# Kernel optimization log

Hardware: AMD Instinct MI355X
Metric: run time of the kernel (lower is better)

Reference implementation:

```python
import jax, jax.numpy as jnp
import numpy as np


def setup_inputs() -> dict:
    key = jax.random.key(0)
    ks = jax.random.split(key, 6)
    B, HW, CIN, COUT, K = 256, 64, 3, 128, 32
    inputs = jax.random.normal(ks[0], (B, HW, HW, CIN), jnp.float32)
    conv_w = jax.random.normal(ks[1], (3, 3, CIN, COUT), jnp.float32) * 0.1
    conv_b = jnp.zeros((COUT,), jnp.float32)
    match_w = jax.random.normal(ks[2], (COUT,), jnp.float32) * 0.1
    match_b = jnp.zeros((1,), jnp.float32)
    pat_w = jax.random.normal(ks[3], (32 * 32 * K, 1), jnp.float32) * 0.01
    pat_b = jnp.zeros((1,), jnp.float32)
    base_w = jax.random.normal(ks[4], (32 * 32 * COUT, 3), jnp.float32) * 0.01
    base_b = jnp.zeros((3,), jnp.float32)
    pattern_set_index = jax.random.randint(ks[5], (K,), 0, COUT, jnp.int32)
    return {
        "inputs": inputs, "conv_w": conv_w, "conv_b": conv_b,
        "match_w": match_w, "match_b": match_b,
        "pat_w": pat_w, "pat_b": pat_b,
        "base_w": base_w, "base_b": base_b,
        "pattern_set_index": pattern_set_index,
    }


def reference(inputs, conv_w, conv_b, match_w, match_b,
              pat_w, pat_b, base_w, base_b, pattern_set_index):
    B = inputs.shape[0]
    # feat_extract: conv3x3 stride 2 + relu -> feats0 [B,32,32,128]; GAP -> feats1 [B,128]
    feats0 = jax.nn.relu(
        jax.lax.conv_general_dilated(
            inputs, conv_w, window_strides=(2, 2), padding='SAME',
            dimension_numbers=('NHWC', 'HWIO', 'NHWC')) + conv_b)
    feats1 = feats0.mean(axis=(1, 2))  # [B,128]
    # pat_matcher: boolean per-sample match mask
    matches = (feats1 @ match_w + match_b[0]) > 0.0  # [B] bool
    # pat_pred on channel-subset features (tf.gather axis=3)
    sel = jnp.take(feats0, pattern_set_index, axis=3)  # [B,32,32,32]
    p = jax.nn.sigmoid(sel.reshape(B, -1) @ pat_w + pat_b)[:, 0]  # [B]
    # BinaryToCategorical(pattern_class=0, num_classes=3): [p, (1-p)/2, (1-p)/2]
    o = (1.0 - p) * 0.5
    cat = jnp.stack([p, o, o], axis=-1)  # [B,3]
    # base_pred on full features (used for matched-low and non-matched samples)
    base = jax.nn.softmax(feats0.reshape(B, -1) @ base_w + base_b, axis=-1)  # [B,3]
    # route: matched AND pat score >= 0.5 -> categorized pat pred, else base pred
    use_pat = matches & (p >= 0.5)
    return jnp.where(use_pat[:, None], cat, base)
```

## Files before the change

### kernel.cpp

```cpp
#include <hip/hip_runtime.h>
#include <math.h>

#define TPB 512

__global__ __launch_bounds__(TPB, 2)
void pattern_branch_kernel(const float* __restrict__ in,
                           const float* __restrict__ conv_w,
                           const float* __restrict__ conv_b,
                           const float* __restrict__ match_w,
                           const float* __restrict__ match_b,
                           const float* __restrict__ pat_w,
                           const float* __restrict__ pat_b,
                           const float* __restrict__ base_w,
                           const float* __restrict__ base_b,
                           const int*   __restrict__ psi,
                           float* __restrict__ out)
{
    constexpr int ROWF4 = 50;
    constexpr int ROWF  = 200;
    __shared__ float4 xlds4[65 * ROWF4];
    __shared__ float  red[8][5];

    const float* xlds = (const float*)xlds4;
    const int b   = blockIdx.x;
    const int tid = threadIdx.x;

    for (int s = tid; s < 65 * ROWF4; s += TPB) xlds4[s] = make_float4(0.f, 0.f, 0.f, 0.f);
    __syncthreads();
    const float4* inp4 = (const float4*)(in + (size_t)b * 12288);
    for (int s = tid; s < 64 * 48; s += TPB) {
        int r = s / 48;
        int q = s - r * 48;
        xlds4[r * ROWF4 + q] = inp4[s];
    }
    __syncthreads();

    const int lane31 = tid & 31;
    const int grp    = tid >> 5;
    float w[4][27], bias[4], mw[4];
    #pragma unroll
    for (int j = 0; j < 4; ++j) {
        int c = lane31 + 32 * j;
        bias[j] = conv_b[c];
        mw[j]   = match_w[c];
        #pragma unroll
        for (int k = 0; k < 27; ++k) w[j][k] = conv_w[k * 128 + c];
    }

    float s_match = 0.f, sb0 = 0.f, sb1 = 0.f, sb2 = 0.f;

    for (int it = 0; it < 16; ++it) {
        int slot = it * 16 + grp;
        int oh = slot >> 3;
        int q  = slot & 7;
        float acc[4][4];
        #pragma unroll
        for (int v = 0; v < 4; ++v)
            #pragma unroll
            for (int j = 0; j < 4; ++j) acc[v][j] = bias[j];

        #pragma unroll
        for (int kh = 0; kh < 3; ++kh) {
            float xr[28];
            const float4* rp = &xlds4[(2 * oh + kh) * ROWF4 + 6 * q];
            #pragma unroll
            for (int u = 0; u < 7; ++u) {
                float4 v4 = rp[u];
                xr[4*u] = v4.x; xr[4*u+1] = v4.y; xr[4*u+2] = v4.z; xr[4*u+3] = v4.w;
            }
            #pragma unroll
            for (int v = 0; v < 4; ++v)
                #pragma unroll
                for (int t9 = 0; t9 < 9; ++t9) {
                    float xv = xr[6 * v + t9];
                    int k = kh * 9 + t9;
                    acc[v][0] = fmaf(xv, w[0][k], acc[v][0]);
                    acc[v][1] = fmaf(xv, w[1][k], acc[v][1]);
                    acc[v][2] = fmaf(xv, w[2][k], acc[v][2]);
                    acc[v][3] = fmaf(xv, w[3][k], acc[v][3]);
                }
        }
        #pragma unroll
        for (int v = 0; v < 4; ++v) {
            int hw = oh * 32 + 4 * q + v;
            const float* bp = base_w + (size_t)(hw * 128 + lane31) * 3;
            #pragma unroll
            for (int j = 0; j < 4; ++j) {
                float fv = fmaxf(acc[v][j], 0.f);
                s_match = fmaf(mw[j], fv, s_match);
                const float* bpj = bp + j * 96;
                sb0 = fmaf(fv, bpj[0], sb0);
                sb1 = fmaf(fv, bpj[1], sb1);
                sb2 = fmaf(fv, bpj[2], sb2);
            }
        }
    }

    float s_pat = 0.f;
    {
        const int lane8 = tid & 7;
        const int pgrp  = tid >> 3;
        int pk[4];
        float pbias[4];
        float pw[4][27];
        #pragma unroll
        for (int j = 0; j < 4; ++j) {
            int k = lane8 + 8 * j;
            pk[j] = k;
            int c = psi[k];
            pbias[j] = conv_b[c];
            #pragma unroll
            for (int kk = 0; kk < 27; ++kk) pw[j][kk] = conv_w[kk * 128 + c];
        }
        for (int it = 0; it < 16; ++it) {
            int hw = it * 64 + pgrp;
            int oh = hw >> 5, ow = hw & 31;
            float a0 = pbias[0], a1 = pbias[1], a2 = pbias[2], a3 = pbias[3];
            #pragma unroll
            for (int kh = 0; kh < 3; ++kh) {
                float xr[10];
                const float2* rp = (const float2*)(xlds + (2 * oh + kh) * ROWF) + 3 * ow;
                #pragma unroll
                for (int u = 0; u < 5; ++u) { float2 v2 = rp[u]; xr[2*u] = v2.x; xr[2*u+1] = v2.y; }
                #pragma unroll
                for (int t9 = 0; t9 < 9; ++t9) {
                    float xv = xr[t9];
                    int k = kh * 9 + t9;
                    a0 = fmaf(xv, pw[0][k], a0);
                    a1 = fmaf(xv, pw[1][k], a1);
                    a2 = fmaf(xv, pw[2][k], a2);
                    a3 = fmaf(xv, pw[3][k], a3);
                }
            }
            const float* pwp = pat_w + hw * 32;
            s_pat = fmaf(fmaxf(a0, 0.f), pwp[pk[0]], s_pat);
            s_pat = fmaf(fmaxf(a1, 0.f), pwp[pk[1]], s_pat);
            s_pat = fmaf(fmaxf(a2, 0.f), pwp[pk[2]], s_pat);
            s_pat = fmaf(fmaxf(a3, 0.f), pwp[pk[3]], s_pat);
        }
    }

    float vals[5] = { s_match, sb0, sb1, sb2, s_pat };
    #pragma unroll
    for (int off = 32; off > 0; off >>= 1)
        #pragma unroll
        for (int v = 0; v < 5; ++v)
            vals[v] += __shfl_down(vals[v], off, 64);
    int wv = tid >> 6, lane = tid & 63;
    if (lane == 0) {
        #pragma unroll
        for (int v = 0; v < 5; ++v) red[wv][v] = vals[v];
    }
    __syncthreads();
    if (tid == 0) {
        float t[5] = {0.f, 0.f, 0.f, 0.f, 0.f};
        for (int wj = 0; wj < 8; ++wj)
            #pragma unroll
            for (int v = 0; v < 5; ++v) t[v] += red[wj][v];
        float score = t[0] * (1.f / 1024.f) + match_b[0];
        float p = 1.f / (1.f + expf(-(t[4] + pat_b[0])));
        float l0 = t[1] + base_b[0], l1 = t[2] + base_b[1], l2 = t[3] + base_b[2];
        float m = fmaxf(l0, fmaxf(l1, l2));
        float e0 = expf(l0 - m), e1 = expf(l1 - m), e2 = expf(l2 - m);
        float inv = 1.f / (e0 + e1 + e2);
        bool use_pat = (score > 0.f) && (p >= 0.5f);
        float o0, o1, o2;
        if (use_pat) { o0 = p; o1 = 0.5f * (1.f - p); o2 = o1; }
        else         { o0 = e0 * inv; o1 = e1 * inv; o2 = e2 * inv; }
        out[b * 3 + 0] = o0;
        out[b * 3 + 1] = o1;
        out[b * 3 + 2] = o2;
    }
}

extern "C" void kernel_launch(void* const* d_in, const int* in_sizes, int n_in,
                              void* d_out, int out_size, void* d_ws, size_t ws_size,
                              hipStream_t stream) {
    const float* in      = (const float*)d_in[0];
    const float* conv_w  = (const float*)d_in[1];
    const float* conv_b  = (const float*)d_in[2];
    const float* match_w = (const float*)d_in[3];
    const float* match_b = (const float*)d_in[4];
    const float* pat_w   = (const float*)d_in[5];
    const float* pat_b   = (const float*)d_in[6];
    const float* base_w  = (const float*)d_in[7];
    const float* base_b  = (const float*)d_in[8];
    const int*   psi     = (const int*)d_in[9];
    float* out = (float*)d_out;

    int B = in_sizes[0] / (64 * 64 * 3);
    pattern_branch_kernel<<<B, TPB, 0, stream>>>(
        in, conv_w, conv_b, match_w, match_b, pat_w, pat_b,
        base_w, base_b, psi, out);
}
```

Measured before the change: 136.8 us.

## Fold pattern gather into per-channel weights and drop duplicate pattern conv

A prep kernel scatters pat_w through pattern_set_index into a dense per-(hw,channel) weight and packs it with the three base_w weights as one float4 per element, written to workspace. The main kernel then computes the pattern logit from the same conv features it already computes, removing the second conv pass over the selected channels. The block also grows to 1024 threads with 2 channels per thread instead of 4. This adds an extra kernel launch each call and doubles thread count, which reduces registers per thread and changes occupancy.

```diff
diff --git a/kernel.cpp b/kernel.cpp
--- a/kernel.cpp
+++ b/kernel.cpp
@@ -1,27 +1,41 @@
 #include <hip/hip_runtime.h>
 #include <math.h>
 
-#define TPB 512
+#define TPB 1024
 
-__global__ __launch_bounds__(TPB, 2)
+__global__ __launch_bounds__(256)
+void prep_weights(const float* __restrict__ base_w,
+                  const float* __restrict__ pat_w,
+                  const int*   __restrict__ psi,
+                  float4* __restrict__ wq)
+{
+    int idx = blockIdx.x * 256 + threadIdx.x;
+    int hw = idx >> 7, c = idx & 127;
+    const float* bp = base_w + (size_t)idx * 3;
+    float b0 = bp[0], b1 = bp[1], b2 = bp[2];
+    float pc = 0.f;
+    const float* pr = pat_w + hw * 32;
+    #pragma unroll
+    for (int k = 0; k < 32; ++k)
+        pc += (psi[k] == c) ? pr[k] : 0.f;
+    wq[idx] = make_float4(b0, b1, b2, pc);
+}
+
+__global__ __launch_bounds__(TPB, 4)
 void pattern_branch_kernel(const float* __restrict__ in,
                            const float* __restrict__ conv_w,
                            const float* __restrict__ conv_b,
                            const float* __restrict__ match_w,
                            const float* __restrict__ match_b,
-                           const float* __restrict__ pat_w,
                            const float* __restrict__ pat_b,
-                           const float* __restrict__ base_w,
                            const float* __restrict__ base_b,
-                           const int*   __restrict__ psi,
+                           const float4* __restrict__ wq,
                            float* __restrict__ out)
 {
     constexpr int ROWF4 = 50;
-    constexpr int ROWF  = 200;
     __shared__ float4 xlds4[65 * ROWF4];
-    __shared__ float  red[8][5];
+    __shared__ float  red[16][5];
 
-    const float* xlds = (const float*)xlds4;
     const int b   = blockIdx.x;
     const int tid = threadIdx.x;
 
@@ -36,28 +50,28 @@
     __syncthreads();
 
     const int lane31 = tid & 31;
-    const int grp    = tid >> 5;
-    float w[4][27], bias[4], mw[4];
+    const int cg     = (tid >> 5) & 1;
+    const int sg     = tid >> 6;
+    const int c0     = lane31 + 32 * cg;
+    float w[2][27], bias[2], mw[2];
     #pragma unroll
-    for (int j = 0; j < 4; ++j) {
-        int c = lane31 + 32 * j;
-        bias[j] = conv_b[c];
-        mw[j]   = match_w[c];
+    for (int jj = 0; jj < 2; ++jj) {
+        int c = c0 + 64 * jj;
+        bias[jj] = conv_b[c];
+        mw[jj]   = match_w[c];
         #pragma unroll
-        for (int k = 0; k < 27; ++k) w[j][k] = conv_w[k * 128 + c];
+        for (int k = 0; k < 27; ++k) w[jj][k] = conv_w[k * 128 + c];
     }
 
-    float s_match = 0.f, sb0 = 0.f, sb1 = 0.f, sb2 = 0.f;
+    float s_match = 0.f, sb0 = 0.f, sb1 = 0.f, sb2 = 0.f, s_pat = 0.f;
 
     for (int it = 0; it < 16; ++it) {
-        int slot = it * 16 + grp;
+        int slot = it * 16 + sg;
         int oh = slot >> 3;
         int q  = slot & 7;
-        float acc[4][4];
+        float acc[4][2];
         #pragma unroll
-        for (int v = 0; v < 4; ++v)
-            #pragma unroll
-            for (int j = 0; j < 4; ++j) acc[v][j] = bias[j];
+        for (int v = 0; v < 4; ++v) { acc[v][0] = bias[0]; acc[v][1] = bias[1]; }
 
         #pragma unroll
         for (int kh = 0; kh < 3; ++kh) {
@@ -76,67 +90,22 @@
                     int k = kh * 9 + t9;
                     acc[v][0] = fmaf(xv, w[0][k], acc[v][0]);
                     acc[v][1] = fmaf(xv, w[1][k], acc[v][1]);
-                    acc[v][2] = fmaf(xv, w[2][k], acc[v][2]);
-                    acc[v][3] = fmaf(xv, w[3][k], acc[v][3]);
                 }
         }
         #pragma unroll
         for (int v = 0; v < 4; ++v) {
             int hw = oh * 32 + 4 * q + v;
-            const float* bp = base_w + (size_t)(hw * 128 + lane31) * 3;
+            const float4* wqp = wq + hw * 128 + c0;
             #pragma unroll
-            for (int j = 0; j < 4; ++j) {
-                float fv = fmaxf(acc[v][j], 0.f);
-                s_match = fmaf(mw[j], fv, s_match);
-                const float* bpj = bp + j * 96;
-                sb0 = fmaf(fv, bpj[0], sb0);
-                sb1 = fmaf(fv, bpj[1], sb1);
-                sb2 = fmaf(fv, bpj[2], sb2);
+            for (int jj = 0; jj < 2; ++jj) {
+                float fv = fmaxf(acc[v][jj], 0.f);
+                float4 wv = wqp[64 * jj];
+                s_match = fmaf(mw[jj], fv, s_match);
+                sb0   = fmaf(fv, wv.x, sb0);
+                sb1   = fmaf(fv, wv.y, sb1);
+                sb2   = fmaf(fv, wv.z, sb2);
+                s_pat = fmaf(fv, wv.w, s_pat);
             }
-        }
-    }
-
-    float s_pat = 0.f;
-    {
-        const int lane8 = tid & 7;
-        const int pgrp  = tid >> 3;
-        int pk[4];
-        float pbias[4];
-        float pw[4][27];
-        #pragma unroll
-        for (int j = 0; j < 4; ++j) {
-            int k = lane8 + 8 * j;
-            pk[j] = k;
-            int c = psi[k];
-            pbias[j] = conv_b[c];
-            #pragma unroll
-            for (int kk = 0; kk < 27; ++kk) pw[j][kk] = conv_w[kk * 128 + c];
-        }
-        for (int it = 0; it < 16; ++it) {
-            int hw = it * 64 + pgrp;
-            int oh = hw >> 5, ow = hw & 31;
-            float a0 = pbias[0], a1 = pbias[1], a2 = pbias[2], a3 = pbias[3];
-            #pragma unroll
-            for (int kh = 0; kh < 3; ++kh) {
-                float xr[10];
-                const float2* rp = (const float2*)(xlds + (2 * oh + kh) * ROWF) + 3 * ow;
-                #pragma unroll
-                for (int u = 0; u < 5; ++u) { float2 v2 = rp[u]; xr[2*u] = v2.x; xr[2*u+1] = v2.y; }
-                #pragma unroll
-                for (int t9 = 0; t9 < 9; ++t9) {
-                    float xv = xr[t9];
-                    int k = kh * 9 + t9;
-                    a0 = fmaf(xv, pw[0][k], a0);
-                    a1 = fmaf(xv, pw[1][k], a1);
-                    a2 = fmaf(xv, pw[2][k], a2);
-                    a3 = fmaf(xv, pw[3][k], a3);
-                }
-            }
-            const float* pwp = pat_w + hw * 32;
-            s_pat = fmaf(fmaxf(a0, 0.f), pwp[pk[0]], s_pat);
-            s_pat = fmaf(fmaxf(a1, 0.f), pwp[pk[1]], s_pat);
-            s_pat = fmaf(fmaxf(a2, 0.f), pwp[pk[2]], s_pat);
-            s_pat = fmaf(fmaxf(a3, 0.f), pwp[pk[3]], s_pat);
         }
     }
 
@@ -154,7 +123,7 @@
     __syncthreads();
     if (tid == 0) {
         float t[5] = {0.f, 0.f, 0.f, 0.f, 0.f};
-        for (int wj = 0; wj < 8; ++wj)
+        for (int wj = 0; wj < 16; ++wj)
             #pragma unroll
             for (int v = 0; v < 5; ++v) t[v] += red[wj][v];
         float score = t[0] * (1.f / 1024.f) + match_b[0];
@@ -188,8 +157,11 @@
     const int*   psi     = (const int*)d_in[9];
     float* out = (float*)d_out;
 
+    float4* wq = (float4*)d_ws;
+
+    prep_weights<<<512, 256, 0, stream>>>(base_w, pat_w, psi, wq);
+
     int B = in_sizes[0] / (64 * 64 * 3);
     pattern_branch_kernel<<<B, TPB, 0, stream>>>(
-        in, conv_w, conv_b, match_w, match_b, pat_w, pat_b,
-        base_w, base_b, psi, out);
+        in, conv_w, conv_b, match_w, match_b, pat_b, base_b, wq, out);
 }
```

Measured after the change: 116.2 us. 1.18x faster.
